# Kernel tuning notes

Measured on AMD Instinct MI355X. Metric: run time of the kernel, lower is better.

Reference implementation:

```python
import jax, jax.numpy as jnp
import numpy as np

NHEAD = 8
NPTS = 4
LN_EPS = 1e-5


def pos_embed(H, W, nf):
    # create_pos_embedding with normalize=True, temperature=10000, scale=2*pi
    scale = 2.0 * np.pi
    eps = 1e-6
    y_e = jnp.arange(1, H + 1, dtype=jnp.float32)
    y_e = y_e / (y_e[-1] + eps) * scale
    x_e = jnp.arange(1, W + 1, dtype=jnp.float32)
    x_e = x_e / (x_e[-1] + eps) * scale
    i = jnp.arange(nf, dtype=jnp.float32)
    dim_t = 10000.0 ** (2.0 * jnp.floor(i / 2.0) / nf)
    def enc(e):
        p = e[:, None] / dim_t  # [len, nf]
        return jnp.stack([jnp.sin(p[:, 0::2]), jnp.cos(p[:, 1::2])], axis=-1).reshape(e.shape[0], -1)
    py = enc(y_e)  # [H, nf]
    px = enc(x_e)  # [W, nf]
    pos = jnp.concatenate([
        jnp.broadcast_to(py[:, None, :], (H, W, nf)),
        jnp.broadcast_to(px[None, :, :], (H, W, nf)),
    ], axis=-1)  # [H, W, 2*nf], channel order (pos_y, pos_x) as in torch cat
    return pos.reshape(H * W, 2 * nf)


def layernorm(x, s, b):
    m = x.mean(-1, keepdims=True)
    v = x.var(-1, keepdims=True)
    return (x - m) * jax.lax.rsqrt(v + LN_EPS) * s + b


def bilinear_sample(value, loc, H, W):
    # value [B, HW, Hd, dh]; loc [B, Q, Hd, P, 2] normalized to [0,1] (x, y)
    # Matches F.grid_sample(align_corners=False, padding_mode='zeros') with grid = 2*loc - 1
    B, HW, Hd, dh = value.shape
    Q = loc.shape[1]
    v = value.transpose(0, 2, 1, 3)  # [B, Hd, HW, dh]
    x = loc[..., 0] * W - 0.5
    y = loc[..., 1] * H - 0.5
    x0 = jnp.floor(x)
    y0 = jnp.floor(y)
    wx1 = x - x0
    wy1 = y - y0
    x0i = x0.astype(jnp.int32)
    y0i = y0.astype(jnp.int32)
    def t(a):  # [B, Q, Hd, P] -> [B, Hd, Q*P]
        return a.transpose(0, 2, 1, 3).reshape(B, Hd, -1)
    def gather(xi, yi):
        valid = ((xi >= 0) & (xi < W) & (yi >= 0) & (yi < H)).astype(v.dtype)
        idx = jnp.clip(yi, 0, H - 1) * W + jnp.clip(xi, 0, W - 1)
        g = jnp.take_along_axis(v, t(idx)[..., None], axis=2)  # [B, Hd, Q*P, dh]
        return g * t(valid)[..., None]
    g00 = gather(x0i, y0i)
    g10 = gather(x0i + 1, y0i)
    g01 = gather(x0i, y0i + 1)
    g11 = gather(x0i + 1, y0i + 1)
    out = (g00 * t((1 - wx1) * (1 - wy1))[..., None]
           + g10 * t(wx1 * (1 - wy1))[..., None]
           + g01 * t((1 - wx1) * wy1)[..., None]
           + g11 * t(wx1 * wy1)[..., None])
    return out.reshape(B, Hd, Q, NPTS, dh)


def _forward(x, merge_w, merge_b, off_w, off_b, aw_w, aw_b, val_w, val_b, out_w, out_b,
             n1_s, n1_b, l1_w, l1_b, l2_w, l2_b, n2_s, n2_b, outc_w, outc_b):
    B, N, C, H, W = x.shape
    D = merge_w.shape[0]
    dh = D // NHEAD
    Q = H * W
    # merge: 1x1 conv + relu
    src = jax.nn.relu(jnp.einsum('bchw,dc->bhwd', x.reshape(B, N * C, H, W), merge_w) + merge_b)
    src = src.reshape(B, Q, D)
    pos = pos_embed(H, W, D // 2)[None].astype(x.dtype)  # [1, Q, D]
    # reference points (valid_ratios = 1): centers of cells, normalized
    ys = (jnp.arange(H, dtype=x.dtype) + 0.5) / H
    xs = (jnp.arange(W, dtype=x.dtype) + 0.5) / W
    gx, gy = jnp.meshgrid(xs, ys, indexing='xy')  # each [H, W]
    ref = jnp.stack([gx, gy], axis=-1).reshape(1, Q, 2)
    norm = jnp.array([W, H], dtype=x.dtype)  # offset normalizer (W, H) for (x, y)
    n_layers = off_w.shape[0]
    for l in range(n_layers):
        q = src + pos
        off = (q @ off_w[l] + off_b[l]).reshape(B, Q, NHEAD, NPTS, 2)
        aw = jax.nn.softmax((q @ aw_w[l] + aw_b[l]).reshape(B, Q, NHEAD, NPTS), axis=-1)
        val = (src @ val_w[l] + val_b[l]).reshape(B, Q, NHEAD, dh)
        loc = ref[:, :, None, None, :] + off / norm  # [B, Q, Hd, P, 2]
        samp = bilinear_sample(val, loc, H, W)  # [B, Hd, Q, P, dh]
        o = (samp * aw.transpose(0, 2, 1, 3)[..., None]).sum(3)  # [B, Hd, Q, dh]
        o = o.transpose(0, 2, 1, 3).reshape(B, Q, D) @ out_w[l] + out_b[l]
        src = layernorm(src + o, n1_s[l], n1_b[l])
        ff = jax.nn.relu(src @ l1_w[l] + l1_b[l]) @ l2_w[l] + l2_b[l]
        src = layernorm(src + ff, n2_s[l], n2_b[l])
    feat = src.reshape(B, H, W, D)
    out = jax.nn.relu(jnp.einsum('bhwc,dc->bhwd', feat, outc_w) + outc_b)
    return out.transpose(0, 3, 1, 2)  # [B, D, H, W]


def setup_inputs() -> dict:
    key = jax.random.key(0)
    B, N, Cb, H, W = 1, 4, 128, 120, 360
    D, Dff, L = 128, 512, 3
    ks = jax.random.split(key, 12)
    def rn(k, shape, s=0.02):
        return jax.random.normal(k, shape, dtype=jnp.float32) * s
    return {
        'x': jax.random.normal(ks[0], (B, N, Cb, H, W), dtype=jnp.float32),
        'merge_w': rn(ks[1], (D, N * Cb)),
        'merge_b': jnp.zeros((D,), jnp.float32),
        'off_w': rn(ks[2], (L, D, NHEAD * NPTS * 2)),
        'off_b': rn(ks[3], (L, NHEAD * NPTS * 2), 0.5),
        'aw_w': rn(ks[4], (L, D, NHEAD * NPTS)),
        'aw_b': jnp.zeros((L, NHEAD * NPTS), jnp.float32),
        'val_w': rn(ks[5], (L, D, D)),
        'val_b': jnp.zeros((L, D), jnp.float32),
        'out_w': rn(ks[6], (L, D, D)),
        'out_b': jnp.zeros((L, D), jnp.float32),
        'n1_s': jnp.ones((L, D), jnp.float32),
        'n1_b': jnp.zeros((L, D), jnp.float32),
        'l1_w': rn(ks[7], (L, D, Dff)),
        'l1_b': jnp.zeros((L, Dff), jnp.float32),
        'l2_w': rn(ks[8], (L, Dff, D)),
        'l2_b': jnp.zeros((L, D), jnp.float32),
        'n2_s': jnp.ones((L, D), jnp.float32),
        'n2_b': jnp.zeros((L, D), jnp.float32),
        'outc_w': rn(ks[9], (D, D)),
        'outc_b': jnp.zeros((D,), jnp.float32),
    }


def reference(x, merge_w, merge_b, off_w, off_b, aw_w, aw_b, val_w, val_b, out_w, out_b,
              n1_s, n1_b, l1_w, l1_b, l2_w, l2_b, n2_s, n2_b, outc_w, outc_b):
    return _forward(x, merge_w, merge_b, off_w, off_b, aw_w, aw_b, val_w, val_b, out_w, out_b,
                    n1_s, n1_b, l1_w, l1_b, l2_w, l2_b, n2_s, n2_b, outc_w, outc_b)
```

## Files before the change

kernel.cpp:

```cpp
#include <hip/hip_runtime.h>
#include <hip/hip_bf16.h>
#include <math.h>

#define Q_TOT 43200
#define H_ 120
#define W_ 360

typedef unsigned short ushort_t;
typedef float f32x4 __attribute__((ext_vector_type(4)));
typedef unsigned short u16x2 __attribute__((ext_vector_type(2)));
typedef unsigned short u16x4 __attribute__((ext_vector_type(4)));
typedef unsigned short u16x8 __attribute__((ext_vector_type(8)));
using short8 = __attribute__((ext_vector_type(8))) short;

static __device__ __forceinline__ float b2f(unsigned short u){
  return __uint_as_float(((unsigned)u) << 16);
}
static __device__ __forceinline__ unsigned short f2b(float f){
  unsigned u = __float_as_uint(f);
  unsigned r = (u + 0x7fffu + ((u >> 16) & 1u)) >> 16;
  return (unsigned short)r;
}

#define SWZ(row, byte) ((byte) ^ (((row) & 7) << 4))
#define SWZ3(row, byte) ((byte) ^ ((((row) ^ ((row) >> 3)) & 7) << 4))

#define CVT_TOT 615072
__global__ __launch_bounds__(256) void cvt_kernel(
    const float* p0, const float* p1, const float* p2, const float* p3,
    const float* p4, const float* p5, const float* p6, const float* p7,
    const float* p8, const float* p9, const float* p10, const float* p11,
    const float* p12, const float* p13, const float* p14, const float* p15,
    const float* p16, const float* p17, const float* p18, const float* p19,
    ushort_t* __restrict__ dst){
  const float* ps[20] = {p0,p1,p2,p3,p4,p5,p6,p7,p8,p9,p10,p11,p12,p13,p14,p15,p16,p17,p18,p19};
  const int offs[20] = {0,65536,65664,90240,90432,102720,102816,151968,152352,201504,
                        201888,202272,202656,399264,400800,597408,597792,598176,598560,614944};
  int gid = blockIdx.x*256 + threadIdx.x;
  if (gid >= CVT_TOT) return;
  int s = 0;
  #pragma unroll
  for (int i=1;i<20;i++) s += (gid >= offs[i]) ? 1 : 0;
  dst[gid] = f2b(ps[s][gid - offs[s]]);
}

#define CVTT_TOT 528384
__global__ __launch_bounds__(256) void cvtT_kernel(
    const float* __restrict__ vw, const float* __restrict__ ow,
    const float* __restrict__ w1, const float* __restrict__ w2,
    const float* __restrict__ offw, const float* __restrict__ aww,
    ushort_t* __restrict__ dst){
  int gid = blockIdx.x*256 + threadIdx.x;
  if (gid >= CVTT_TOT) return;
  if (gid >= 491520){
    int e = gid - 491520;
    int l = e / 12288, rem = e - l*12288;
    int n = rem >> 7, k = rem & 127;
    float v = (n < 64) ? offw[((size_t)l*128 + k)*64 + n]
                       : aww [((size_t)l*128 + k)*32 + (n-64)];
    dst[gid] = f2b(v);
    return;
  }
  const float* s; int K, N, off;
  if (gid < 49152)      { s = vw; K = 128; N = 128; off = 0; }
  else if (gid < 98304) { s = ow; K = 128; N = 128; off = 49152; }
  else if (gid < 294912){ s = w1; K = 128; N = 512; off = 98304; }
  else                  { s = w2; K = 512; N = 128; off = 294912; }
  int e = gid - off;
  int per = K*N;
  int l = e / per, rem = e - l*per;
  int n = rem / K, k = rem - n*K;
  dst[gid] = f2b(s[(size_t)l*per + (size_t)k*N + n]);
}

__global__ __launch_bounds__(256) void postab_kernel(float* __restrict__ tab){
  int gid = blockIdx.x*256 + threadIdx.x;
  if (gid >= 480*64) return;
  int row = gid >> 6, k = gid & 63;
  int m = k >> 1;
  float t = powf(10000.0f, (float)m * (1.0f/32.0f));
  float e;
  if (row < 120) e = (float)(row+1)   * (6.283185307179586f/((float)H_+1e-6f));
  else           e = (float)(row-119) * (6.283185307179586f/((float)W_+1e-6f));
  float p = e / t;
  tab[gid] = (k & 1) ? cosf(p) : sinf(p);
}

__global__ __launch_bounds__(256, 6) void merge_mfma(const float* __restrict__ x,
    const ushort_t* __restrict__ mw,
    const ushort_t* __restrict__ mb,
    ushort_t* __restrict__ srcbf){
  __shared__ ushort_t xt[2][32*128];
  const int tid = threadIdx.x;
  const int wave = tid >> 6, lane = tid & 63;
  const int lr = lane & 15, kg = lane >> 4;
  const int q0 = blockIdx.x * 32;
  const int qq4 = (tid & 7) * 4;
  const int c4  = (tid >> 3) * 4;
  const int qh = wave & 1, dq = wave >> 1;
  const int qrow = qh*16 + lr;

  f32x4 v[4];
  #pragma unroll
  for (int cc=0;cc<4;cc++)
    v[cc] = *(const f32x4*)(x + (size_t)(c4 + cc)*Q_TOT + q0 + qq4);
  #pragma unroll
  for (int qq=0;qq<4;qq++){
    int row = qq4 + qq;
    u16x4 pk;
    #pragma unroll
    for (int cc=0;cc<4;cc++) pk[cc] = f2b(v[cc][qq]);
    *(u16x4*)((char*)xt[0] + SWZ3(row, row*256 + c4*2)) = pk;
  }
  __syncthreads();

  f32x4 acc[4];
  #pragma unroll
  for (int i=0;i<4;i++) acc[i] = (f32x4){0.f,0.f,0.f,0.f};

  for (int ch = 0; ch < 4; ch++){
    f32x4 v2[4];
    if (ch < 3){
      #pragma unroll
      for (int cc=0;cc<4;cc++)
        v2[cc] = *(const f32x4*)(x + (size_t)((ch+1)*128 + c4 + cc)*Q_TOT + q0 + qq4);
    }
    const ushort_t* xb = xt[ch & 1];
    short8 xfc[4];
    #pragma unroll
    for (int ks=0; ks<4; ks++)
      xfc[ks] = *(const short8*)((const char*)xb + SWZ3(qrow, qrow*256 + (ks*32 + kg*8)*2));
    short8 wfr[2][4];
    #pragma unroll
    for (int ks=0; ks<4; ks++)
      wfr[0][ks] = *(const short8*)(mw + (size_t)(dq*64 + lr)*512 + ch*128 + ks*32 + kg*8);
    #pragma unroll
    for (int dtl=0; dtl<4; dtl++){
      if (dtl < 3){
        const int nr = (dq*4 + dtl+1)*16 + lr;
        #pragma unroll
        for (int ks=0; ks<4; ks++)
          wfr[(dtl+1)&1][ks] = *(const short8*)(mw + (size_t)nr*512 + ch*128 + ks*32 + kg*8);
      }
      #pragma unroll
      for (int ks=0; ks<4; ks++)
        acc[dtl] = __builtin_amdgcn_mfma_f32_16x16x32_bf16(xfc[ks], wfr[dtl&1][ks], acc[dtl], 0, 0, 0);
    }
    if (ch < 3){
      ushort_t* xn = xt[(ch+1) & 1];
      #pragma unroll
      for (int qq=0;qq<4;qq++){
        int row = qq4 + qq;
        u16x4 pk;
        #pragma unroll
        for (int cc=0;cc<4;cc++) pk[cc] = f2b(v2[cc][qq]);
        *(u16x4*)((char*)xn + SWZ3(row, row*256 + c4*2)) = pk;
      }
      __syncthreads();
    }
  }
  #pragma unroll
  for (int dtl=0; dtl<4; dtl++){
    int d = (dq*4 + dtl)*16 + lr;
    float bb = b2f(mb[d]);
    #pragma unroll
    for (int r=0; r<4; r++){
      int q = q0 + qh*16 + kg*4 + r;
      float vv = acc[dtl][r] + bb;
      srcbf[(size_t)q*128 + d] = f2b(vv > 0.f ? vv : 0.f);
    }
  }
}

__global__ __launch_bounds__(256, 3) void qv_mfma(const ushort_t* __restrict__ srcbf,
    const float* __restrict__ py, const float* __restrict__ px,
    const ushort_t* __restrict__ owt,
    const ushort_t* __restrict__ ob, const ushort_t* __restrict__ awb,
    const ushort_t* __restrict__ vwt,
    const ushort_t* __restrict__ vb,
    float* __restrict__ loc, float* __restrict__ awg,
    ushort_t* __restrict__ valbf){
  __shared__ ushort_t a_lds[64*128];
  __shared__ ushort_t qlds[64*128];
  const int tid = threadIdx.x;
  const int wave = tid >> 6, lane = tid & 63;
  const int lr = lane & 15, kg = lane >> 4;
  const int q0 = blockIdx.x * 64;
  #pragma unroll
  for (int i=0;i<4;i++){
    int idx = i*256 + tid;
    int row = idx >> 4, ch = idx & 15;
    int q = q0 + row, qy = q / W_, qx = q - qy*W_;
    u16x8 s = *(const u16x8*)(srcbf + (size_t)q*128 + ch*8);
    int c0 = ch*8;
    const float* tp = (c0 < 64) ? (py + qy*64 + c0) : (px + qx*64 + (c0-64));
    f32x4 t0 = *(const f32x4*)tp, t1 = *(const f32x4*)(tp+4);
    u16x8 pq;
    #pragma unroll
    for (int j=0;j<4;j++){
      pq[j]   = f2b(b2f(s[j])   + t0[j]);
      pq[4+j] = f2b(b2f(s[4+j]) + t1[j]);
    }
    int byte = row*256 + c0*2;
    *(u16x8*)((char*)a_lds + SWZ(row, byte)) = s;
    *(u16x8*)((char*)qlds + SWZ(row, byte)) = pq;
  }
  __syncthreads();
  const int qrow = wave*16 + lr;
  short8 xf[4], xq[4];
  #pragma unroll
  for (int ks=0; ks<4; ks++){
    xf[ks] = *(const short8*)((const char*)a_lds + SWZ(qrow, qrow*256 + (ks*32+kg*8)*2));
    xq[ks] = *(const short8*)((const char*)qlds + SWZ(qrow, qrow*256 + (ks*32+kg*8)*2));
  }
  f32x4 va[8];
  #pragma unroll
  for (int dt=0; dt<8; dt++) va[dt] = (f32x4){0.f,0.f,0.f,0.f};
  short8 yf[2][4];
  #pragma unroll
  for (int ks=0; ks<4; ks++)
    yf[0][ks] = *(const short8*)(vwt + (size_t)lr*128 + ks*32 + kg*8);
  #pragma unroll
  for (int dt=0; dt<8; dt++){
    if (dt < 7){
      const int nr = (dt+1)*16 + lr;
      #pragma unroll
      for (int ks=0; ks<4; ks++)
        yf[(dt+1)&1][ks] = *(const short8*)(vwt + (size_t)nr*128 + ks*32 + kg*8);
    }
    #pragma unroll
    for (int ks=0; ks<4; ks++)
      va[dt] = __builtin_amdgcn_mfma_f32_16x16x32_bf16(xf[ks], yf[dt&1][ks], va[dt], 0, 0, 0);
  }
  f32x4 qa[6];
  #pragma unroll
  for (int nt=0; nt<6; nt++) qa[nt] = (f32x4){0.f,0.f,0.f,0.f};
  short8 of[2][4];
  #pragma unroll
  for (int ks=0; ks<4; ks++)
    of[0][ks] = *(const short8*)(owt + (size_t)lr*128 + ks*32 + kg*8);
  #pragma unroll
  for (int nt=0; nt<6; nt++){
    if (nt < 5){
      const int nr = (nt+1)*16 + lr;
      #pragma unroll
      for (int ks=0; ks<4; ks++)
        of[(nt+1)&1][ks] = *(const short8*)(owt + (size_t)nr*128 + ks*32 + kg*8);
    }
    #pragma unroll
    for (int ks=0; ks<4; ks++)
      qa[nt] = __builtin_amdgcn_mfma_f32_16x16x32_bf16(xq[ks], of[nt&1][ks], qa[nt], 0, 0, 0);
  }
  #pragma unroll
  for (int dt=0; dt<8; dt++){
    float bb = b2f(vb[dt*16 + lr]);
    #pragma unroll
    for (int r=0; r<4; r++){
      int q = q0 + wave*16 + kg*4 + r;
      valbf[(size_t)q*128 + dt*16 + lr] = f2b(va[dt][r] + bb);
    }
  }
  #pragma unroll
  for (int r=0; r<4; r++){
    int q = q0 + wave*16 + kg*4 + r;
    int qy = q / W_, qx = q - qy*W_;
    float qxf = (float)qx, qyf = (float)qy;
    #pragma unroll
    for (int dt=0; dt<4; dt++){
      int n = dt*16 + lr;
      float v = qa[dt][r] + b2f(ob[n]);
      loc[(size_t)q*64 + n] = ((n & 1) ? qyf : qxf) + v;
    }
    #pragma unroll
    for (int d4=0; d4<2; d4++){
      int idx = d4*16 + lr;
      float v = qa[4+d4][r] + b2f(awb[idx]);
      float mx = fmaxf(v, __shfl_xor(v, 1, 64));
      mx = fmaxf(mx, __shfl_xor(mx, 2, 64));
      float e = expf(v - mx);
      float s = e + __shfl_xor(e, 1, 64);
      s = s + __shfl_xor(s, 2, 64);
      awg[(size_t)q*32 + idx] = e / s;
    }
  }
}

__global__ __launch_bounds__(256) void sample_kernel(const ushort_t* __restrict__ val,
    const float* __restrict__ loc, const float* __restrict__ awg,
    ushort_t* __restrict__ obf){
  __shared__ float sl[4][64];
  __shared__ float sa[4][32];
  const int tid = threadIdx.x;
  const int q0 = blockIdx.x * 4;
  sl[0][tid & 255] = loc[(size_t)q0*64 + tid];
  if (tid < 128) sa[0][tid] = awg[(size_t)q0*32 + tid];
  __syncthreads();
  const int ql = tid >> 6, cp = (tid & 63) * 2;
  const int h = cp >> 4;
  float a0 = 0.f, a1 = 0.f;
  #pragma unroll
  for (int p=0;p<4;p++){
    float x = sl[ql][h*8 + p*2];
    float y = sl[ql][h*8 + p*2 + 1];
    float wgt = sa[ql][h*4 + p];
    float x0f = floorf(x), y0f = floorf(y);
    float wx = x - x0f, wy = y - y0f;
    int ix = (int)x0f, iy = (int)y0f;
    int x0c = min(max(ix, 0), W_-1),   x1c = min(max(ix+1, 0), W_-1);
    int y0c = min(max(iy, 0), H_-1),   y1c = min(max(iy+1, 0), H_-1);
    float vx0 = (ix   >= 0 && ix   < W_) ? 1.f : 0.f;
    float vx1 = (ix+1 >= 0 && ix+1 < W_) ? 1.f : 0.f;
    float vy0 = (iy   >= 0 && iy   < H_) ? 1.f : 0.f;
    float vy1 = (iy+1 >= 0 && iy+1 < H_) ? 1.f : 0.f;
    float w00 = (1.f-wx)*(1.f-wy)*vx0*vy0 * wgt;
    float w10 = wx*(1.f-wy)*vx1*vy0 * wgt;
    float w01 = (1.f-wx)*wy*vx0*vy1 * wgt;
    float w11 = wx*wy*vx1*vy1 * wgt;
    unsigned g00 = *(const unsigned*)(val + (size_t)(y0c*W_ + x0c)*128 + cp);
    unsigned g10 = *(const unsigned*)(val + (size_t)(y0c*W_ + x1c)*128 + cp);
    unsigned g01 = *(const unsigned*)(val + (size_t)(y1c*W_ + x0c)*128 + cp);
    unsigned g11 = *(const unsigned*)(val + (size_t)(y1c*W_ + x1c)*128 + cp);
    a0 += w00*b2f((ushort_t)g00) + w10*b2f((ushort_t)g10)
        + w01*b2f((ushort_t)g01) + w11*b2f((ushort_t)g11);
    a1 += w00*b2f((ushort_t)(g00>>16)) + w10*b2f((ushort_t)(g10>>16))
        + w01*b2f((ushort_t)(g01>>16)) + w11*b2f((ushort_t)(g11>>16));
  }
  unsigned pk = (unsigned)f2b(a0) | ((unsigned)f2b(a1) << 16);
  *(unsigned*)&obf[(size_t)(q0+ql)*128 + cp] = pk;
}

__global__ __launch_bounds__(256, 3) void outln_mfma(const ushort_t* __restrict__ obf,
    const ushort_t* __restrict__ wt,
    const ushort_t* __restrict__ bias,
    const ushort_t* __restrict__ gs, const ushort_t* __restrict__ gb,
    ushort_t* srcbf){
  __shared__ ushort_t a_lds[64*128];
  const int tid = threadIdx.x;
  const int wave = tid >> 6, lane = tid & 63;
  const int lr = lane & 15, kg = lane >> 4;
  const int q0 = blockIdx.x * 64;
  #pragma unroll
  for (int i=0;i<4;i++){
    int idx = i*256 + tid;
    int row = idx >> 4, ch = idx & 15;
    u16x8 s = *(const u16x8*)(obf + (size_t)(q0+row)*128 + ch*8);
    *(u16x8*)((char*)a_lds + SWZ(row, row*256 + ch*16)) = s;
  }
  __syncthreads();
  const int qrow = wave*16 + lr;
  short8 xf[4];
  #pragma unroll
  for (int ks=0; ks<4; ks++)
    xf[ks] = *(const short8*)((const char*)a_lds + SWZ(qrow, qrow*256 + (ks*32+kg*8)*2));
  f32x4 acc[8];
  #pragma unroll
  for (int dt=0; dt<8; dt++) acc[dt] = (f32x4){0.f,0.f,0.f,0.f};
  short8 yf[2][4];
  #pragma unroll
  for (int ks=0; ks<4; ks++)
    yf[0][ks] = *(const short8*)(wt + (size_t)lr*128 + ks*32 + kg*8);
  #pragma unroll
  for (int dt=0; dt<8; dt++){
    if (dt < 7){
      const int nr = (dt+1)*16 + lr;
      #pragma unroll
      for (int ks=0; ks<4; ks++)
        yf[(dt+1)&1][ks] = *(const short8*)(wt + (size_t)nr*128 + ks*32 + kg*8);
    }
    #pragma unroll
    for (int ks=0; ks<4; ks++)
      acc[dt] = __builtin_amdgcn_mfma_f32_16x16x32_bf16(xf[ks], yf[dt&1][ks], acc[dt], 0, 0, 0);
  }
  float g4[8], be4[8], bi4[8];
  #pragma unroll
  for (int dt=0; dt<8; dt++){
    g4[dt] = b2f(gs[dt*16+lr]); be4[dt] = b2f(gb[dt*16+lr]); bi4[dt] = b2f(bias[dt*16+lr]);
  }
  #pragma unroll
  for (int r=0; r<4; r++){
    const int q = q0 + wave*16 + kg*4 + r;
    float vals[8];
    float s1 = 0.f, s2 = 0.f;
    #pragma unroll
    for (int dt=0; dt<8; dt++){
      float v = acc[dt][r] + bi4[dt] + b2f(srcbf[(size_t)q*128 + dt*16 + lr]);
      vals[dt] = v; s1 += v; s2 += v*v;
    }
    #pragma unroll
    for (int m=1; m<16; m<<=1){ s1 += __shfl_xor(s1, m, 64); s2 += __shfl_xor(s2, m, 64); }
    float mean = s1*(1.f/128.f);
    float var  = s2*(1.f/128.f) - mean*mean;
    float inv  = rsqrtf(var + 1e-5f);
    #pragma unroll
    for (int dt=0; dt<8; dt++)
      srcbf[(size_t)q*128 + dt*16 + lr] = f2b((vals[dt]-mean)*inv*g4[dt] + be4[dt]);
  }
}

__global__ __launch_bounds__(512, 4) void ffn_mfma(
    const ushort_t* __restrict__ w1t,
    const ushort_t* __restrict__ b1,
    const ushort_t* __restrict__ w2t,
    const ushort_t* __restrict__ b2,
    const ushort_t* __restrict__ gs, const ushort_t* __restrict__ gb,
    ushort_t* srcbf){
  __shared__ char smem[49152];
  ushort_t* a_lds = (ushort_t*)smem;
  ushort_t* h_lds = (ushort_t*)(smem + 16384);
  float* scr = (float*)smem;
  const int tid = threadIdx.x;
  const int wave = tid >> 6, lane = tid & 63;
  const int lr = lane & 15, kg = lane >> 4;
  const int q0 = blockIdx.x * 64;
  #pragma unroll
  for (int i=0;i<2;i++){
    int idx = i*512 + tid;
    int row = idx >> 4, ch = idx & 15;
    u16x8 s = *(const u16x8*)(srcbf + (size_t)(q0+row)*128 + ch*8);
    *(u16x8*)((char*)a_lds + SWZ(row, row*256 + ch*16)) = s;
  }
  const int drow = wave*16 + lr;
  f32x4 accd[4];
  #pragma unroll
  for (int qt=0; qt<4; qt++) accd[qt] = (f32x4){0.f,0.f,0.f,0.f};
  __syncthreads();
  for (int half=0; half<2; half++){
    short8 wf[2][4];
    #pragma unroll
    for (int nt=0; nt<2; nt++){
      const int nrow = (half*16 + wave*2 + nt)*16 + lr;
      #pragma unroll
      for (int ks=0; ks<4; ks++)
        wf[nt][ks] = *(const short8*)(w1t + (size_t)nrow*128 + ks*32 + kg*8);
    }
    short8 yg[8];
    #pragma unroll
    for (int ks=0; ks<8; ks++)
      yg[ks] = *(const short8*)(w2t + (size_t)drow*512 + half*256 + ks*32 + kg*8);
    #pragma unroll
    for (int nt=0; nt<2; nt++){
      const int ngt = half*16 + wave*2 + nt;
      u16x4 bb = *(const u16x4*)(b1 + ngt*16 + kg*4);
      float bf[4];
      #pragma unroll
      for (int j=0;j<4;j++) bf[j] = b2f(bb[j]);
      #pragma unroll
      for (int qt=0; qt<4; qt++){
        f32x4 acc = (f32x4){0.f,0.f,0.f,0.f};
        const int q = qt*16 + lr;
        #pragma unroll
        for (int ks=0; ks<4; ks++){
          short8 yf = *(const short8*)((const char*)a_lds + SWZ(q, q*256 + (ks*32 + kg*8)*2));
          acc = __builtin_amdgcn_mfma_f32_16x16x32_bf16(wf[nt][ks], yf, acc, 0, 0, 0);
        }
        const int nl = (ngt & 15)*16 + kg*4;
        u16x4 hp;
        #pragma unroll
        for (int r=0;r<4;r++){ float v = acc[r] + bf[r]; hp[r] = f2b(v > 0.f ? v : 0.f); }
        *(u16x4*)((char*)h_lds + SWZ(q, q*512 + nl*2)) = hp;
      }
    }
    __syncthreads();
    #pragma unroll
    for (int qt=0; qt<4; qt++){
      const int qrow = qt*16 + lr;
      short8 xh[8];
      #pragma unroll
      for (int ks=0; ks<8; ks++)
        xh[ks] = *(const short8*)((const char*)h_lds + SWZ(qrow, qrow*512 + (ks*32 + kg*8)*2));
      #pragma unroll
      for (int ks=0; ks<8; ks++)
        accd[qt] = __builtin_amdgcn_mfma_f32_16x16x32_bf16(xh[ks], yg[ks], accd[qt], 0, 0, 0);
    }
    __syncthreads();
  }
  #pragma unroll
  for (int qt=0; qt<4; qt++)
    #pragma unroll
    for (int r=0; r<4; r++)
      scr[(qt*16 + kg*4 + r)*132 + wave*16 + lr] = accd[qt][r];
  __syncthreads();
  {
    const int c = lane*2;
    float bi0 = b2f(b2[c]),  bi1 = b2f(b2[c+1]);
    float g0  = b2f(gs[c]),  g1  = b2f(gs[c+1]);
    float be0 = b2f(gb[c]),  be1 = b2f(gb[c+1]);
    #pragma unroll
    for (int i=0; i<8; i++){
      const int ql = wave*8 + i;
      unsigned rr = *(const unsigned*)(srcbf + (size_t)(q0+ql)*128 + c);
      float v0 = scr[ql*132 + c]     + bi0 + b2f((ushort_t)rr);
      float v1 = scr[ql*132 + c + 1] + bi1 + b2f((ushort_t)(rr >> 16));
      float s1 = v0 + v1, s2 = v0*v0 + v1*v1;
      #pragma unroll
      for (int m=1; m<64; m<<=1){ s1 += __shfl_xor(s1, m, 64); s2 += __shfl_xor(s2, m, 64); }
      float mean = s1*(1.f/128.f);
      float var  = s2*(1.f/128.f) - mean*mean;
      float inv  = rsqrtf(var + 1e-5f);
      float o0 = (v0-mean)*inv*g0 + be0;
      float o1 = (v1-mean)*inv*g1 + be1;
      unsigned pk = (unsigned)f2b(o0) | ((unsigned)f2b(o1) << 16);
      *(unsigned*)(srcbf + (size_t)(q0+ql)*128 + c) = pk;
    }
  }
}

__global__ __launch_bounds__(256, 3) void outc_mfma(const ushort_t* __restrict__ srcbf,
    const ushort_t* __restrict__ wt,
    const ushort_t* __restrict__ bias,
    float* __restrict__ outp){
  __shared__ ushort_t a_lds[64*128];
  const int tid = threadIdx.x;
  const int wave = tid >> 6, lane = tid & 63;
  const int lr = lane & 15, kg = lane >> 4;
  const int q0 = blockIdx.x * 64;
  #pragma unroll
  for (int i=0;i<4;i++){
    int idx = i*256 + tid;
    int row = idx >> 4, ch = idx & 15;
    u16x8 s = *(const u16x8*)(srcbf + (size_t)(q0+row)*128 + ch*8);
    *(u16x8*)((char*)a_lds + SWZ(row, row*256 + ch*16)) = s;
  }
  __syncthreads();
  const int qrow = wave*16 + lr;
  short8 xf[4];
  #pragma unroll
  for (int ks=0; ks<4; ks++)
    xf[ks] = *(const short8*)((const char*)a_lds + SWZ(qrow, qrow*256 + (ks*32+kg*8)*2));
  f32x4 acc[8];
  #pragma unroll
  for (int dt=0; dt<8; dt++) acc[dt] = (f32x4){0.f,0.f,0.f,0.f};
  short8 yf[2][4];
  #pragma unroll
  for (int ks=0; ks<4; ks++)
    yf[0][ks] = *(const short8*)(wt + (size_t)lr*128 + ks*32 + kg*8);
  #pragma unroll
  for (int dt=0; dt<8; dt++){
    if (dt < 7){
      const int nr = (dt+1)*16 + lr;
      #pragma unroll
      for (int ks=0; ks<4; ks++)
        yf[(dt+1)&1][ks] = *(const short8*)(wt + (size_t)nr*128 + ks*32 + kg*8);
    }
    #pragma unroll
    for (int ks=0; ks<4; ks++)
      acc[dt] = __builtin_amdgcn_mfma_f32_16x16x32_bf16(xf[ks], yf[dt&1][ks], acc[dt], 0, 0, 0);
  }
  #pragma unroll
  for (int dt=0; dt<8; dt++){
    float bb = b2f(bias[dt*16 + lr]);
    #pragma unroll
    for (int r=0; r<4; r++){
      int q = q0 + wave*16 + kg*4 + r;
      float v = acc[dt][r] + bb;
      v = v > 0.f ? v : 0.f;
      outp[(size_t)(dt*16 + lr)*Q_TOT + q] = v;
    }
  }
}

extern "C" void kernel_launch(void* const* d_in, const int* in_sizes, int n_in,
                              void* d_out, int out_size, void* d_ws, size_t ws_size,
                              hipStream_t stream){
  const float* x = (const float*)d_in[0];

  ushort_t* srcbf = (ushort_t*)d_ws;
  ushort_t* obf   = srcbf + (size_t)Q_TOT*128;
  ushort_t* valbf = obf   + (size_t)Q_TOT*128;
  float* loc = (float*)(valbf + (size_t)Q_TOT*128);
  float* aw  = loc + (size_t)Q_TOT*64;
  ushort_t* wbf   = (ushort_t*)(aw + (size_t)Q_TOT*32);
  ushort_t* tbase = wbf + 615072;
  float* postab = (float*)(tbase + 528384);
  float* pytab = postab;
  float* pxtab = postab + 120*64;

  const ushort_t* mw     = wbf + 0;
  const ushort_t* mb     = wbf + 65536;
  const ushort_t* off_b  = wbf + 90240;
  const ushort_t* aw_b   = wbf + 102720;
  const ushort_t* val_b  = wbf + 151968;
  const ushort_t* out_b  = wbf + 201504;
  const ushort_t* n1_s   = wbf + 201888;
  const ushort_t* n1_b   = wbf + 202272;
  const ushort_t* l1_b   = wbf + 399264;
  const ushort_t* l2_b   = wbf + 597408;
  const ushort_t* n2_s   = wbf + 597792;
  const ushort_t* n2_b   = wbf + 598176;
  const ushort_t* outc_w = wbf + 598560;
  const ushort_t* outc_b = wbf + 614944;
  const ushort_t* val_wt = tbase + 0;
  const ushort_t* out_wt = tbase + 49152;
  const ushort_t* l1_wt  = tbase + 98304;
  const ushort_t* l2_wt  = tbase + 294912;
  const ushort_t* oaw_t  = tbase + 491520;

  cvt_kernel<<<(CVT_TOT+255)/256, 256, 0, stream>>>(
      (const float*)d_in[1],  (const float*)d_in[2],  (const float*)d_in[3],
      (const float*)d_in[4],  (const float*)d_in[5],  (const float*)d_in[6],
      (const float*)d_in[7],  (const float*)d_in[8],  (const float*)d_in[9],
      (const float*)d_in[10], (const float*)d_in[11], (const float*)d_in[12],
      (const float*)d_in[13], (const float*)d_in[14], (const float*)d_in[15],
      (const float*)d_in[16], (const float*)d_in[17], (const float*)d_in[18],
      (const float*)d_in[19], (const float*)d_in[20], wbf);
  cvtT_kernel<<<CVTT_TOT/256, 256, 0, stream>>>(
      (const float*)d_in[7], (const float*)d_in[9],
      (const float*)d_in[13], (const float*)d_in[15],
      (const float*)d_in[3], (const float*)d_in[5], tbase);
  postab_kernel<<<120, 256, 0, stream>>>(postab);

  merge_mfma<<<Q_TOT/32, 256, 0, stream>>>(x, mw, mb, srcbf);
  for (int l = 0; l < 3; l++){
    qv_mfma<<<Q_TOT/64, 256, 0, stream>>>(srcbf, pytab, pxtab,
        oaw_t + (size_t)l*96*128, off_b + (size_t)l*64, aw_b + (size_t)l*32,
        val_wt + (size_t)l*128*128, val_b + (size_t)l*128,
        loc, aw, valbf);
    sample_kernel<<<Q_TOT/4, 256, 0, stream>>>(valbf, loc, aw, obf);
    outln_mfma<<<Q_TOT/64, 256, 0, stream>>>(obf,
        out_wt + (size_t)l*128*128, out_b + (size_t)l*128,
        n1_s + (size_t)l*128, n1_b + (size_t)l*128, srcbf);
    ffn_mfma<<<Q_TOT/64, 512, 0, stream>>>(
        l1_wt + (size_t)l*512*128, l1_b + (size_t)l*512,
        l2_wt + (size_t)l*128*512, l2_b + (size_t)l*128,
        n2_s + (size_t)l*128, n2_b + (size_t)l*128, srcbf);
  }
  outc_mfma<<<Q_TOT/64, 256, 0, stream>>>(srcbf, outc_w, outc_b, (float*)d_out);
}
```

Before: 384.3 us.

## Split merge into transpose-to-bf16 pass and larger-tile MFMA GEMM

Adds a separate kernel that transposes the channel-major fp32 input into a query-major bf16 buffer through shared memory. The merge GEMM then reads contiguous bf16 rows, uses 64-query tiles with 8 waves each owning 16 output channels, and keeps weight fragments in registers across query tiles. The aim is coalesced input reads, less conversion work inside the GEMM, and more weight reuse. In exchange it adds an extra kernel launch and a full write and read of the intermediate bf16 buffer in workspace.

```diff
diff --git a/kernel.cpp b/kernel.cpp
--- a/kernel.cpp
+++ b/kernel.cpp
@@ -23,7 +23,6 @@
 }
 
 #define SWZ(row, byte) ((byte) ^ (((row) & 7) << 4))
-#define SWZ3(row, byte) ((byte) ^ ((((row) ^ ((row) >> 3)) & 7) << 4))
 
 #define CVT_TOT 615072
 __global__ __launch_bounds__(256) void cvt_kernel(
@@ -86,88 +85,97 @@
   tab[gid] = (k & 1) ? cosf(p) : sinf(p);
 }
 
-__global__ __launch_bounds__(256, 6) void merge_mfma(const float* __restrict__ x,
+__global__ __launch_bounds__(256) void xT_kernel(const float* __restrict__ x,
+    ushort_t* __restrict__ xbf){
+  __shared__ float t[32][65];
+  const int tid = threadIdx.x;
+  const int qt = blockIdx.x >> 4, ct = blockIdx.x & 15;
+  const int q0 = qt * 64, c0 = ct * 32;
+  {
+    int row = tid >> 3, qoff = (tid & 7) * 8;
+    const float* sp = x + (size_t)(c0 + row)*Q_TOT + q0 + qoff;
+    f32x4 a = *(const f32x4*)sp;
+    f32x4 b = *(const f32x4*)(sp + 4);
+    #pragma unroll
+    for (int j=0;j<4;j++){ t[row][qoff+j] = a[j]; t[row][qoff+4+j] = b[j]; }
+  }
+  __syncthreads();
+  {
+    int qrow = tid >> 2, cseg = (tid & 3) * 8;
+    u16x8 pk;
+    #pragma unroll
+    for (int j=0;j<8;j++) pk[j] = f2b(t[cseg+j][qrow]);
+    *(u16x8*)(xbf + (size_t)(q0 + qrow)*512 + c0 + cseg) = pk;
+  }
+}
+
+__global__ __launch_bounds__(512, 3) void merge_mfma(const ushort_t* __restrict__ xbf,
     const ushort_t* __restrict__ mw,
     const ushort_t* __restrict__ mb,
     ushort_t* __restrict__ srcbf){
-  __shared__ ushort_t xt[2][32*128];
+  __shared__ ushort_t a_lds[2][64*128];
   const int tid = threadIdx.x;
   const int wave = tid >> 6, lane = tid & 63;
   const int lr = lane & 15, kg = lane >> 4;
-  const int q0 = blockIdx.x * 32;
-  const int qq4 = (tid & 7) * 4;
-  const int c4  = (tid >> 3) * 4;
-  const int qh = wave & 1, dq = wave >> 1;
-  const int qrow = qh*16 + lr;
-
-  f32x4 v[4];
-  #pragma unroll
-  for (int cc=0;cc<4;cc++)
-    v[cc] = *(const f32x4*)(x + (size_t)(c4 + cc)*Q_TOT + q0 + qq4);
-  #pragma unroll
-  for (int qq=0;qq<4;qq++){
-    int row = qq4 + qq;
-    u16x4 pk;
-    #pragma unroll
-    for (int cc=0;cc<4;cc++) pk[cc] = f2b(v[cc][qq]);
-    *(u16x4*)((char*)xt[0] + SWZ3(row, row*256 + c4*2)) = pk;
-  }
-  __syncthreads();
-
+  const int q0 = blockIdx.x * 64;
+  const int drow = wave*16 + lr;
+  #pragma unroll
+  for (int i=0;i<2;i++){
+    int idx = i*512 + tid;
+    int row = idx >> 4, ch = idx & 15;
+    u16x8 s = *(const u16x8*)(xbf + (size_t)(q0+row)*512 + ch*8);
+    *(u16x8*)((char*)a_lds[0] + SWZ(row, row*256 + ch*16)) = s;
+  }
+  __syncthreads();
   f32x4 acc[4];
   #pragma unroll
-  for (int i=0;i<4;i++) acc[i] = (f32x4){0.f,0.f,0.f,0.f};
-
+  for (int qt=0; qt<4; qt++) acc[qt] = (f32x4){0.f,0.f,0.f,0.f};
   for (int ch = 0; ch < 4; ch++){
-    f32x4 v2[4];
+    u16x8 st[2];
     if (ch < 3){
       #pragma unroll
-      for (int cc=0;cc<4;cc++)
-        v2[cc] = *(const f32x4*)(x + (size_t)((ch+1)*128 + c4 + cc)*Q_TOT + q0 + qq4);
-    }
-    const ushort_t* xb = xt[ch & 1];
-    short8 xfc[4];
+      for (int i=0;i<2;i++){
+        int idx = i*512 + tid;
+        int row = idx >> 4, cc = idx & 15;
+        st[i] = *(const u16x8*)(xbf + (size_t)(q0+row)*512 + (ch+1)*128 + cc*8);
+      }
+    }
+    short8 wf[4];
     #pragma unroll
     for (int ks=0; ks<4; ks++)
-      xfc[ks] = *(const short8*)((const char*)xb + SWZ3(qrow, qrow*256 + (ks*32 + kg*8)*2));
-    short8 wfr[2][4];
-    #pragma unroll
-    for (int ks=0; ks<4; ks++)
-      wfr[0][ks] = *(const short8*)(mw + (size_t)(dq*64 + lr)*512 + ch*128 + ks*32 + kg*8);
-    #pragma unroll
-    for (int dtl=0; dtl<4; dtl++){
-      if (dtl < 3){
-        const int nr = (dq*4 + dtl+1)*16 + lr;
-        #pragma unroll
-        for (int ks=0; ks<4; ks++)
-          wfr[(dtl+1)&1][ks] = *(const short8*)(mw + (size_t)nr*512 + ch*128 + ks*32 + kg*8);
-      }
+      wf[ks] = *(const short8*)(mw + (size_t)drow*512 + ch*128 + ks*32 + kg*8);
+    const ushort_t* xb = a_lds[ch & 1];
+    #pragma unroll
+    for (int qt=0; qt<4; qt++){
+      const int qrow = qt*16 + lr;
+      short8 xf[4];
       #pragma unroll
       for (int ks=0; ks<4; ks++)
-        acc[dtl] = __builtin_amdgcn_mfma_f32_16x16x32_bf16(xfc[ks], wfr[dtl&1][ks], acc[dtl], 0, 0, 0);
+        xf[ks] = *(const short8*)((const char*)xb + SWZ(qrow, qrow*256 + (ks*32 + kg*8)*2));
+      #pragma unroll
+      for (int ks=0; ks<4; ks++)
+        acc[qt] = __builtin_amdgcn_mfma_f32_16x16x32_bf16(xf[ks], wf[ks], acc[qt], 0, 0, 0);
     }
     if (ch < 3){
-      ushort_t* xn = xt[(ch+1) & 1];
-      #pragma unroll
-      for (int qq=0;qq<4;qq++){
-        int row = qq4 + qq;
-        u16x4 pk;
-        #pragma unroll
-        for (int cc=0;cc<4;cc++) pk[cc] = f2b(v2[cc][qq]);
-        *(u16x4*)((char*)xn + SWZ3(row, row*256 + c4*2)) = pk;
+      ushort_t* xn = a_lds[(ch+1) & 1];
+      #pragma unroll
+      for (int i=0;i<2;i++){
+        int idx = i*512 + tid;
+        int row = idx >> 4, cc = idx & 15;
+        *(u16x8*)((char*)xn + SWZ(row, row*256 + cc*16)) = st[i];
       }
       __syncthreads();
     }
   }
-  #pragma unroll
-  for (int dtl=0; dtl<4; dtl++){
-    int d = (dq*4 + dtl)*16 + lr;
-    float bb = b2f(mb[d]);
+  float bb = b2f(mb[drow]);
+  #pragma unroll
+  for (int qt=0; qt<4; qt++){
     #pragma unroll
     for (int r=0; r<4; r++){
-      int q = q0 + qh*16 + kg*4 + r;
-      float vv = acc[dtl][r] + bb;
-      srcbf[(size_t)q*128 + d] = f2b(vv > 0.f ? vv : 0.f);
+      int q = q0 + qt*16 + kg*4 + r;
+      float vv = acc[qt][r] + bb;
+      srcbf[(size_t)q*128 + drow] = f2b(vv > 0.f ? vv : 0.f);
+      (void)0;
     }
   }
 }
@@ -574,6 +582,7 @@
   float* postab = (float*)(tbase + 528384);
   float* pytab = postab;
   float* pxtab = postab + 120*64;
+  ushort_t* xbf = (ushort_t*)(postab + 480*64);
 
   const ushort_t* mw     = wbf + 0;
   const ushort_t* mb     = wbf + 65536;
@@ -609,7 +618,8 @@
       (const float*)d_in[3], (const float*)d_in[5], tbase);
   postab_kernel<<<120, 256, 0, stream>>>(postab);
 
-  merge_mfma<<<Q_TOT/32, 256, 0, stream>>>(x, mw, mb, srcbf);
+  xT_kernel<<<(Q_TOT/64)*16, 256, 0, stream>>>(x, xbf);
+  merge_mfma<<<Q_TOT/64, 512, 0, stream>>>(xbf, mw, mb, srcbf);
   for (int l = 0; l < 3; l++){
     qv_mfma<<<Q_TOT/64, 256, 0, stream>>>(srcbf, pytab, pxtab,
         oaw_t + (size_t)l*96*128, off_b + (size_t)l*64, aw_b + (size_t)l*32,
```

After: 382.6 us. Within noise of the previous version (-0.4%).
